# Kernel optimization log

Measured on AMD Instinct MI355X. Metric: run time of the kernel, lower is better.

## Reference

```python
import jax, jax.numpy as jnp
import numpy as np

N = 100000   # nodes
E = 1600000  # edges (avg degree 16)
IN = 64
HID = 16     # hardcoded in ChebNet.conv1
OUT = 40
K = 3


def setup_inputs() -> dict:
    key = jax.random.key(0)
    k0, k1, k2, k3 = jax.random.split(key, 4)
    x = jax.random.normal(k0, (N, IN), jnp.float32)
    edge_index = jax.random.randint(k1, (2, E), 0, N, jnp.int32)
    # Glorot-style init for the K per-order linear maps of each ChebConv
    s1 = float(np.sqrt(2.0 / (IN + HID)))
    W1 = jax.random.normal(k2, (K, IN, HID), jnp.float32) * s1
    b1 = jnp.zeros((HID,), jnp.float32)
    s2 = float(np.sqrt(2.0 / (HID + OUT)))
    W2 = jax.random.normal(k3, (K, HID, OUT), jnp.float32) * s2
    b2 = jnp.zeros((OUT,), jnp.float32)
    return {"x": x, "edge_index": edge_index, "W1": W1, "b1": b1, "W2": W2, "b2": b2}


def cheb_conv(x, edge_index, W, b):
    """PyG ChebConv with normalization='sym', lambda_max=2.
    Scaled Laplacian: L_hat = 2L/lambda_max - I = -D^{-1/2} A D^{-1/2} (diag 0).
    out = sum_k T_k(L_hat) x @ W[k] + b, T0=x, T1=L_hat x, Tk=2 L_hat T_{k-1}-T_{k-2}.
    """
    row, col = edge_index[0], edge_index[1]
    ones = jnp.ones((edge_index.shape[1],), x.dtype)
    deg = jax.ops.segment_sum(ones, row, num_segments=N)
    dis = jnp.where(deg > 0, jax.lax.rsqrt(jnp.maximum(deg, 1.0)), 0.0)
    norm = -(dis[row] * dis[col])  # [E]

    def Lhat(z):  # sparse scatter-gather: gather src rows, scale, scatter-add to dst
        return jax.ops.segment_sum(norm[:, None] * z[row], col, num_segments=N)

    Tx0 = x
    out = Tx0 @ W[0]
    Tx1 = Lhat(x)
    if W.shape[0] > 1:
        out = out + Tx1 @ W[1]
    for k in range(2, W.shape[0]):
        Tx2 = 2.0 * Lhat(Tx1) - Tx0
        out = out + Tx2 @ W[k]
        Tx0, Tx1 = Tx1, Tx2
    return out + b


def reference(x, edge_index, W1, b1, W2, b2):
    h = jax.nn.relu(cheb_conv(x, edge_index, W1, b1))
    h = cheb_conv(h, edge_index, W2, b2)
    return jax.nn.log_softmax(h, axis=1)
```

## Files before the change

### kernel.cpp

```cpp
#include <hip/hip_runtime.h>
#include <hip/hip_bf16.h>


typedef unsigned short u16;

constexpr int N_    = 100000;
constexpr int E_    = 1600000;
constexpr int IN_   = 64;
constexpr int HID_  = 16;
constexpr int OUT_  = 40;
constexpr int CAP_  = 48;
constexpr int S_    = 64;
constexpr int EPS_  = E_ / S_;
constexpr int P4_   = 4;
constexpr int NPP4_ = N_ / P4_;
constexpr int P8_   = 8;
constexpr int NPP8_ = N_ / P8_;
constexpr int NPAD_ = 100352;

__device__ __forceinline__ float bf2f(u16 u) {
    return __uint_as_float((unsigned)u << 16);
}
__device__ __forceinline__ u16 f2bf(float x) {
    unsigned u = __float_as_uint(x);
    return (u16)((u + 0x7FFFu + ((u >> 16) & 1u)) >> 16);
}

__global__ void __launch_bounds__(1024)
hist2(const int* __restrict__ row, const int* __restrict__ col,
      u16* __restrict__ prow, u16* __restrict__ pcol) {
    __shared__ int lds[NPP4_];
    if (blockIdx.x < P4_ * S_) {
        int p = blockIdx.x & 3, s = blockIdx.x >> 2;
        for (int i = threadIdx.x; i < NPP4_; i += 1024) lds[i] = 0;
        __syncthreads();
        int lo = p * NPP4_, e0 = s * EPS_;
        for (int i = threadIdx.x; i < EPS_; i += 1024) {
            int c = col[e0 + i];
            unsigned d = (unsigned)(c - lo);
            if (d < (unsigned)NPP4_) atomicAdd(&lds[d], 1);
        }
        __syncthreads();
        u16* dst = pcol + (size_t)(p * S_ + s) * NPP4_;
        for (int i = threadIdx.x; i < NPP4_; i += 1024) dst[i] = (u16)lds[i];
    } else {
        int b = blockIdx.x - P4_ * S_;
        int p = b & 7, s = b >> 3;
        for (int i = threadIdx.x; i < NPP8_; i += 1024) lds[i] = 0;
        __syncthreads();
        int lo = p * NPP8_, e0 = s * EPS_;
        for (int i = threadIdx.x; i < EPS_; i += 1024) {
            int r = row[e0 + i];
            unsigned d = (unsigned)(r - lo);
            if (d < (unsigned)NPP8_) atomicAdd(&lds[d], 1);
        }
        __syncthreads();
        u16* dst = prow + (size_t)(p * S_ + s) * NPP8_;
        for (int i = threadIdx.x; i < NPP8_; i += 1024) dst[i] = (u16)lds[i];
    }
}

__global__ void __launch_bounds__(1024)
reduce_all(const u16* __restrict__ prow, const u16* __restrict__ pcol,
           float* __restrict__ dis, u16* __restrict__ pre, int* __restrict__ indeg) {
    int n = blockIdx.x * 1024 + threadIdx.x;
    if (n >= N_) return;
    {
        int p = n / NPP8_, i = n - p * NPP8_;
        const u16* base = prow + (size_t)(p * S_) * NPP8_ + i;
        int d = 0;
#pragma unroll 8
        for (int s = 0; s < S_; ++s) d += base[(size_t)s * NPP8_];
        dis[n] = (d > 0) ? rsqrtf((float)d) : 0.0f;
    }
    {
        int p = n / NPP4_, i = n - p * NPP4_;
        const u16* base = pcol + (size_t)(p * S_) * NPP4_ + i;
        int run = 0;
#pragma unroll 8
        for (int s = 0; s < S_; ++s) {
            pre[(size_t)s * NPAD_ + n] = (u16)run;
            run += base[(size_t)s * NPP4_];
        }
        indeg[n] = run;
    }
}

__global__ void __launch_bounds__(1024)
place_proj(const int* __restrict__ row, const int* __restrict__ col,
           const float* __restrict__ x, const float* __restrict__ W,
           const float* __restrict__ dis, const u16* __restrict__ pre,
           int* __restrict__ bucket,
           float* __restrict__ P0f, float* __restrict__ P2f,
           u16* __restrict__ A1, u16* __restrict__ A2) {
    __shared__ int pos[NPP4_];
    __shared__ float w[3 * IN_ * HID_];
    if (blockIdx.x < P4_ * S_) {
        int p = blockIdx.x & 3, s = blockIdx.x >> 2;
        int lo = p * NPP4_, e0 = s * EPS_;
        const u16* psrc = pre + (size_t)s * NPAD_ + lo;
        for (int i = threadIdx.x; i < NPP4_; i += 1024) pos[i] = psrc[i];
        __syncthreads();
        for (int i = threadIdx.x; i < EPS_; i += 1024) {
            int c = col[e0 + i];
            unsigned d = (unsigned)(c - lo);
            if (d < (unsigned)NPP4_) {
                int r = row[e0 + i];
                int q = atomicAdd(&pos[d], 1);
                if (q < CAP_) bucket[(size_t)c * CAP_ + q] = r;
            }
        }
    } else {
        for (int i = threadIdx.x; i < 3 * IN_ * HID_; i += 1024) w[i] = W[i];
        __syncthreads();
        int t = (blockIdx.x - P4_ * S_) * 1024 + threadIdx.x;
        if (t >= N_ * HID_) return;
        int n = t >> 4, j = t & 15;
        const float* xr = x + (size_t)n * IN_;
        float a0 = 0.f, a1 = 0.f, a2 = 0.f;
#pragma unroll
        for (int i = 0; i < IN_; ++i) {
            float xv = xr[i];
            a0 += xv * w[i * 16 + j];
            a1 += xv * w[1024 + i * 16 + j];
            a2 += xv * w[2048 + i * 16 + j];
        }
        float dn = dis[n];
        P0f[t] = a0;
        P2f[t] = a2;
        A1[t] = f2bf(dn * a1);
        A2[t] = f2bf(dn * a2);
    }
}

__global__ void g32b(const u16* __restrict__ A1, const u16* __restrict__ A2,
                     const int* __restrict__ indeg, const int* __restrict__ bucket,
                     const float* __restrict__ dis,
                     float* __restrict__ LP1f, u16* __restrict__ B2) {
    int wib = threadIdx.x >> 6, lane = threadIdx.x & 63;
    int n0 = (blockIdx.x * 4 + wib) * 4;
    int eg = lane >> 3, sub = lane & 7;
    const u16* Z = (sub < 4) ? A1 : A2;
    int fq = sub & 3;
    int4 mi = *(const int4*)&indeg[n0];
    int m[4] = {min(mi.x, CAP_), min(mi.y, CAP_), min(mi.z, CAP_), min(mi.w, CAP_)};
    int mmax = max(max(m[0], m[1]), max(m[2], m[3]));
    float ax[4] = {0,0,0,0}, ay[4] = {0,0,0,0}, az[4] = {0,0,0,0}, aw[4] = {0,0,0,0};
    for (int base = 0; base < mmax; base += 8) {
        int e = base + eg;
        int rr[4]; float vm[4];
#pragma unroll
        for (int k = 0; k < 4; ++k) {
            bool v = e < m[k];
            rr[k] = bucket[(size_t)(n0 + k) * CAP_ + (v ? e : 0)];
            vm[k] = v ? 1.0f : 0.0f;
        }
#pragma unroll
        for (int k = 0; k < 4; ++k) {
            int r = (vm[k] != 0.0f) ? rr[k] : 0;
            ushort4 zv = *(const ushort4*)&Z[(size_t)r * 16 + fq * 4];
            ax[k] += vm[k] * bf2f(zv.x); ay[k] += vm[k] * bf2f(zv.y);
            az[k] += vm[k] * bf2f(zv.z); aw[k] += vm[k] * bf2f(zv.w);
        }
    }
#pragma unroll
    for (int off = 8; off < 64; off <<= 1) {
#pragma unroll
        for (int k = 0; k < 4; ++k) {
            ax[k] += __shfl_xor(ax[k], off, 64); ay[k] += __shfl_xor(ay[k], off, 64);
            az[k] += __shfl_xor(az[k], off, 64); aw[k] += __shfl_xor(aw[k], off, 64);
        }
    }
    if (lane < 8) {
#pragma unroll
        for (int k = 0; k < 4; ++k) {
            int n = n0 + k;
            float dn = dis[n];
            if (lane < 4) {
                float4 v = {-dn * ax[k], -dn * ay[k], -dn * az[k], -dn * aw[k]};
                *(float4*)&LP1f[(size_t)n * 16 + fq * 4] = v;
            } else {
                float s = -(dn * dn);
                ushort4 v = {f2bf(s * ax[k]), f2bf(s * ay[k]),
                             f2bf(s * az[k]), f2bf(s * aw[k])};
                *(ushort4*)&B2[(size_t)n * 16 + fq * 4] = v;
            }
        }
    }
}

__device__ __forceinline__ void g16core4(const u16* __restrict__ Z,
                                         const int* __restrict__ indeg,
                                         const int* __restrict__ bucket,
                                         int n0, int lane, float4 acc[4]) {
    int eg = lane >> 2, fq = lane & 3;
    int4 mi = *(const int4*)&indeg[n0];
    int m[4] = {min(mi.x, CAP_), min(mi.y, CAP_), min(mi.z, CAP_), min(mi.w, CAP_)};
    int mmax = max(max(m[0], m[1]), max(m[2], m[3]));
    float ax[4] = {0,0,0,0}, ay[4] = {0,0,0,0}, az[4] = {0,0,0,0}, aw[4] = {0,0,0,0};
    for (int base = 0; base < mmax; base += 16) {
        int e = base + eg;
        int rr[4]; float vm[4];
#pragma unroll
        for (int k = 0; k < 4; ++k) {
            bool v = e < m[k];
            rr[k] = bucket[(size_t)(n0 + k) * CAP_ + (v ? e : 0)];
            vm[k] = v ? 1.0f : 0.0f;
        }
#pragma unroll
        for (int k = 0; k < 4; ++k) {
            int r = (vm[k] != 0.0f) ? rr[k] : 0;
            ushort4 zv = *(const ushort4*)&Z[(size_t)r * 16 + fq * 4];
            ax[k] += vm[k] * bf2f(zv.x); ay[k] += vm[k] * bf2f(zv.y);
            az[k] += vm[k] * bf2f(zv.z); aw[k] += vm[k] * bf2f(zv.w);
        }
    }
#pragma unroll
    for (int off = 4; off < 64; off <<= 1) {
#pragma unroll
        for (int k = 0; k < 4; ++k) {
            ax[k] += __shfl_xor(ax[k], off, 64); ay[k] += __shfl_xor(ay[k], off, 64);
            az[k] += __shfl_xor(az[k], off, 64); aw[k] += __shfl_xor(aw[k], off, 64);
        }
    }
#pragma unroll
    for (int k = 0; k < 4; ++k) {
        float4 r4 = {ax[k], ay[k], az[k], aw[k]};
        acc[k] = r4;
    }
}

__global__ void g16_combine(const u16* __restrict__ B2, const int* __restrict__ indeg,
                            const int* __restrict__ bucket, const float* __restrict__ dis,
                            const float* __restrict__ LP1f, const float* __restrict__ P2f,
                            const float* __restrict__ b1,
                            float* p0h , u16* __restrict__ Hs) {
    int wib = threadIdx.x >> 6, lane = threadIdx.x & 63;
    int n0 = (blockIdx.x * 4 + wib) * 4;
    float4 acc[4];
    g16core4(B2, indeg, bucket, n0, lane, acc);
    if (lane < 4) {
#pragma unroll
        for (int k = 0; k < 4; ++k) {
            int n = n0 + k;
            float dn = dis[n];
            float4 p0 = *(const float4*)&p0h[(size_t)n * 16 + lane * 4];
            float4 lp = *(const float4*)&LP1f[(size_t)n * 16 + lane * 4];
            float4 p2 = *(const float4*)&P2f[(size_t)n * 16 + lane * 4];
            float4 bb = *(const float4*)&b1[lane * 4];
            float4 hv;
            hv.x = fmaxf(p0.x + lp.x - 2.f * dn * acc[k].x - p2.x + bb.x, 0.f);
            hv.y = fmaxf(p0.y + lp.y - 2.f * dn * acc[k].y - p2.y + bb.y, 0.f);
            hv.z = fmaxf(p0.z + lp.z - 2.f * dn * acc[k].z - p2.z + bb.z, 0.f);
            hv.w = fmaxf(p0.w + lp.w - 2.f * dn * acc[k].w - p2.w + bb.w, 0.f);
            *(float4*)&p0h[(size_t)n * 16 + lane * 4] = hv;
            ushort4 hs = {f2bf(dn * hv.x), f2bf(dn * hv.y),
                          f2bf(dn * hv.z), f2bf(dn * hv.w)};
            *(ushort4*)&Hs[(size_t)n * 16 + lane * 4] = hs;
        }
    }
}

__global__ void g16_t1(const u16* __restrict__ Hs, const int* __restrict__ indeg,
                       const int* __restrict__ bucket, const float* __restrict__ dis,
                       float* __restrict__ T1f, u16* __restrict__ Ts) {
    int wib = threadIdx.x >> 6, lane = threadIdx.x & 63;
    int n0 = (blockIdx.x * 4 + wib) * 4;
    float4 acc[4];
    g16core4(Hs, indeg, bucket, n0, lane, acc);
    if (lane < 4) {
#pragma unroll
        for (int k = 0; k < 4; ++k) {
            int n = n0 + k;
            float dn = dis[n];
            float4 t1 = {-dn * acc[k].x, -dn * acc[k].y, -dn * acc[k].z, -dn * acc[k].w};
            *(float4*)&T1f[(size_t)n * 16 + lane * 4] = t1;
            ushort4 ts = {f2bf(dn * t1.x), f2bf(dn * t1.y),
                          f2bf(dn * t1.z), f2bf(dn * t1.w)};
            *(ushort4*)&Ts[(size_t)n * 16 + lane * 4] = ts;
        }
    }
}

__global__ void g16_t2(const u16* __restrict__ Ts, const int* __restrict__ indeg,
                       const int* __restrict__ bucket, const float* __restrict__ dis,
                       const float* __restrict__ Hf, float* __restrict__ T2f) {
    int wib = threadIdx.x >> 6, lane = threadIdx.x & 63;
    int n0 = (blockIdx.x * 4 + wib) * 4;
    float4 acc[4];
    g16core4(Ts, indeg, bucket, n0, lane, acc);
    if (lane < 4) {
#pragma unroll
        for (int k = 0; k < 4; ++k) {
            int n = n0 + k;
            float dn = dis[n];
            float4 h4 = *(const float4*)&Hf[(size_t)n * 16 + lane * 4];
            float4 t2;
            t2.x = -2.f * dn * acc[k].x - h4.x;
            t2.y = -2.f * dn * acc[k].y - h4.y;
            t2.z = -2.f * dn * acc[k].z - h4.z;
            t2.w = -2.f * dn * acc[k].w - h4.w;
            *(float4*)&T2f[(size_t)n * 16 + lane * 4] = t2;
        }
    }
}

__global__ void __launch_bounds__(256)
mm2_lsm(const float* __restrict__ Hf, const float* __restrict__ T1f,
        const float* __restrict__ T2f, const float* __restrict__ W2,
        const float* __restrict__ b2, float* __restrict__ out) {
    int n = blockIdx.x * 256 + threadIdx.x;
    if (n >= N_) return;
    float act[48];
#pragma unroll
    for (int q = 0; q < 4; ++q)
        *(float4*)&act[q * 4] = *(const float4*)&Hf[(size_t)n * 16 + q * 4];
#pragma unroll
    for (int q = 0; q < 4; ++q)
        *(float4*)&act[16 + q * 4] = *(const float4*)&T1f[(size_t)n * 16 + q * 4];
#pragma unroll
    for (int q = 0; q < 4; ++q)
        *(float4*)&act[32 + q * 4] = *(const float4*)&T2f[(size_t)n * 16 + q * 4];
    float acc[OUT_];
#pragma unroll
    for (int o = 0; o < OUT_; ++o) acc[o] = b2[o];
#pragma unroll
    for (int j = 0; j < HID_; ++j) {
        float a0 = act[j], a1 = act[16 + j], a2 = act[32 + j];
#pragma unroll
        for (int o = 0; o < OUT_; ++o) {
            acc[o] += a0 * W2[j * OUT_ + o]
                    + a1 * W2[640 + j * OUT_ + o]
                    + a2 * W2[1280 + j * OUT_ + o];
        }
    }
    float mx = acc[0];
#pragma unroll
    for (int o = 1; o < OUT_; ++o) mx = fmaxf(mx, acc[o]);
    float s = 0.f;
#pragma unroll
    for (int o = 0; o < OUT_; ++o) s += __expf(acc[o] - mx);
    float ls = mx + logf(s);
#pragma unroll
    for (int q = 0; q < 10; ++q) {
        float4 v = {acc[q * 4] - ls, acc[q * 4 + 1] - ls,
                    acc[q * 4 + 2] - ls, acc[q * 4 + 3] - ls};
        *(float4*)&out[(size_t)n * OUT_ + q * 4] = v;
    }
}


extern "C" void kernel_launch(void* const* d_in, const int* in_sizes, int n_in,
                              void* d_out, int out_size, void* d_ws, size_t ws_size,
                              hipStream_t stream) {
    const float* x  = (const float*)d_in[0];
    const int*   ei = (const int*)d_in[1];
    const float* W1 = (const float*)d_in[2];
    const float* b1 = (const float*)d_in[3];
    const float* W2 = (const float*)d_in[4];
    const float* b2 = (const float*)d_in[5];
    float* out = (float*)d_out;

    const int* row = ei;
    const int* col = ei + E_;

    char* wp = (char*)d_ws;
    float* dis    = (float*)wp;  wp += 401408;
    int*   indeg  = (int*)wp;    wp += 401408;
    int*   bucket = (int*)wp;    wp += (size_t)N_ * CAP_ * 4;
    u16*   pre    = (u16*)wp;    wp += (size_t)S_ * NPAD_ * 2;
    char*  region = wp;
    u16* pcol = (u16*)region;
    u16* prow = (u16*)(region + 12800000);
    wp = region;
    u16*   A1   = (u16*)wp;   wp += 3211264;
    u16*   A2   = (u16*)wp;   wp += 3211264;
    u16*   B2   = (u16*)wp;   wp += 3211264;
    float* P0f  = (float*)wp; wp += 6422528;
    float* P2f  = (float*)wp; wp += 6422528;
    float* LP1f = (float*)wp; wp += 6422528;

    float* Hf  = P0f;
    u16*   Hs  = A1;
    float* T1f = LP1f;
    u16*   Ts  = A2;
    float* T2f = P2f;

    hist2<<<P4_ * S_ + P8_ * S_, 1024, 0, stream>>>(row, col, prow, pcol);
    reduce_all<<<NPAD_ / 1024, 1024, 0, stream>>>(prow, pcol, dis, pre, indeg);
    place_proj<<<P4_ * S_ + 1563, 1024, 0, stream>>>(row, col, x, W1, dis, pre,
                                                     bucket, P0f, P2f, A1, A2);

    g32b<<<N_ / 16, 256, 0, stream>>>(A1, A2, indeg, bucket, dis, LP1f, B2);
    g16_combine<<<N_ / 16, 256, 0, stream>>>(B2, indeg, bucket, dis, LP1f, P2f, b1,
                                             P0f , Hs);
    g16_t1<<<N_ / 16, 256, 0, stream>>>(Hs, indeg, bucket, dis, T1f, Ts);
    g16_t2<<<N_ / 16, 256, 0, stream>>>(Ts, indeg, bucket, dis, Hf, T2f);
    mm2_lsm<<<(N_ + 255) / 256, 256, 0, stream>>>(Hf, T1f, T2f, W2, b2, out);
}
```

Before: 313.7 us.

## Unify row/col histogram partitioning and interleave bucket placement with projection blocks

The row-degree histogram now uses the same 4-way node partition as the column histogram, so hist2 has a single code path and launches 512 blocks instead of 768. In place_proj, bucket-placement blocks and projection blocks are interleaved by block index (bit 2 of blockIdx selects the role), so the slow atomic scatter blocks are spread across the grid instead of all sitting at the front. The weight buffer reuses the pos LDS array rather than declaring a separate shared array. The aim is better load balance and occupancy. The cost is 3128 launched blocks with some exiting early, plus fewer, larger per-block histograms for the row pass.

New measurement: 317.3 us. About the same (+1.2%).

```diff
diff --git a/kernel.cpp b/kernel.cpp
--- a/kernel.cpp
+++ b/kernel.cpp
@@ -14,9 +14,8 @@
 constexpr int EPS_  = E_ / S_;
 constexpr int P4_   = 4;
 constexpr int NPP4_ = N_ / P4_;
-constexpr int P8_   = 8;
-constexpr int NPP8_ = N_ / P8_;
 constexpr int NPAD_ = 100352;
+constexpr int PROJB_ = 1563;
 
 __device__ __forceinline__ float bf2f(u16 u) {
     return __uint_as_float((unsigned)u << 16);
@@ -30,34 +29,22 @@
 hist2(const int* __restrict__ row, const int* __restrict__ col,
       u16* __restrict__ prow, u16* __restrict__ pcol) {
     __shared__ int lds[NPP4_];
-    if (blockIdx.x < P4_ * S_) {
-        int p = blockIdx.x & 3, s = blockIdx.x >> 2;
-        for (int i = threadIdx.x; i < NPP4_; i += 1024) lds[i] = 0;
-        __syncthreads();
-        int lo = p * NPP4_, e0 = s * EPS_;
-        for (int i = threadIdx.x; i < EPS_; i += 1024) {
-            int c = col[e0 + i];
-            unsigned d = (unsigned)(c - lo);
-            if (d < (unsigned)NPP4_) atomicAdd(&lds[d], 1);
-        }
-        __syncthreads();
-        u16* dst = pcol + (size_t)(p * S_ + s) * NPP4_;
-        for (int i = threadIdx.x; i < NPP4_; i += 1024) dst[i] = (u16)lds[i];
-    } else {
-        int b = blockIdx.x - P4_ * S_;
-        int p = b & 7, s = b >> 3;
-        for (int i = threadIdx.x; i < NPP8_; i += 1024) lds[i] = 0;
-        __syncthreads();
-        int lo = p * NPP8_, e0 = s * EPS_;
-        for (int i = threadIdx.x; i < EPS_; i += 1024) {
-            int r = row[e0 + i];
-            unsigned d = (unsigned)(r - lo);
-            if (d < (unsigned)NPP8_) atomicAdd(&lds[d], 1);
-        }
-        __syncthreads();
-        u16* dst = prow + (size_t)(p * S_ + s) * NPP8_;
-        for (int i = threadIdx.x; i < NPP8_; i += 1024) dst[i] = (u16)lds[i];
-    }
+    bool isCol = blockIdx.x < P4_ * S_;
+    int b = isCol ? blockIdx.x : (blockIdx.x - P4_ * S_);
+    const int* arr = isCol ? col : row;
+    u16* dstbase = isCol ? pcol : prow;
+    int p = b & 3, s = b >> 2;
+    for (int i = threadIdx.x; i < NPP4_; i += 1024) lds[i] = 0;
+    __syncthreads();
+    int lo = p * NPP4_, e0 = s * EPS_;
+    for (int i = threadIdx.x; i < EPS_; i += 1024) {
+        int v = arr[e0 + i];
+        unsigned d = (unsigned)(v - lo);
+        if (d < (unsigned)NPP4_) atomicAdd(&lds[d], 1);
+    }
+    __syncthreads();
+    u16* dst = dstbase + (size_t)(p * S_ + s) * NPP4_;
+    for (int i = threadIdx.x; i < NPP4_; i += 1024) dst[i] = (u16)lds[i];
 }
 
 __global__ void __launch_bounds__(1024)
@@ -65,16 +52,15 @@
            float* __restrict__ dis, u16* __restrict__ pre, int* __restrict__ indeg) {
     int n = blockIdx.x * 1024 + threadIdx.x;
     if (n >= N_) return;
+    int p = n / NPP4_, i = n - p * NPP4_;
     {
-        int p = n / NPP8_, i = n - p * NPP8_;
-        const u16* base = prow + (size_t)(p * S_) * NPP8_ + i;
+        const u16* base = prow + (size_t)(p * S_) * NPP4_ + i;
         int d = 0;
 #pragma unroll 8
-        for (int s = 0; s < S_; ++s) d += base[(size_t)s * NPP8_];
+        for (int s = 0; s < S_; ++s) d += base[(size_t)s * NPP4_];
         dis[n] = (d > 0) ? rsqrtf((float)d) : 0.0f;
     }
     {
-        int p = n / NPP4_, i = n - p * NPP4_;
         const u16* base = pcol + (size_t)(p * S_) * NPP4_ + i;
         int run = 0;
 #pragma unroll 8
@@ -94,9 +80,11 @@
            float* __restrict__ P0f, float* __restrict__ P2f,
            u16* __restrict__ A1, u16* __restrict__ A2) {
     __shared__ int pos[NPP4_];
-    __shared__ float w[3 * IN_ * HID_];
-    if (blockIdx.x < P4_ * S_) {
-        int p = blockIdx.x & 3, s = blockIdx.x >> 2;
+    float* w = (float*)pos;
+    if ((blockIdx.x & 4) == 0) {
+        int s = (int)(blockIdx.x >> 3);
+        if (s >= S_) return;
+        int p = blockIdx.x & 3;
         int lo = p * NPP4_, e0 = s * EPS_;
         const u16* psrc = pre + (size_t)s * NPAD_ + lo;
         for (int i = threadIdx.x; i < NPP4_; i += 1024) pos[i] = psrc[i];
@@ -111,19 +99,21 @@
             }
         }
     } else {
+        int j = (int)(blockIdx.x >> 3) * 4 + (int)(blockIdx.x & 3);
+        if (j >= PROJB_) return;
         for (int i = threadIdx.x; i < 3 * IN_ * HID_; i += 1024) w[i] = W[i];
         __syncthreads();
-        int t = (blockIdx.x - P4_ * S_) * 1024 + threadIdx.x;
+        int t = j * 1024 + threadIdx.x;
         if (t >= N_ * HID_) return;
-        int n = t >> 4, j = t & 15;
+        int n = t >> 4, jj = t & 15;
         const float* xr = x + (size_t)n * IN_;
         float a0 = 0.f, a1 = 0.f, a2 = 0.f;
 #pragma unroll
         for (int i = 0; i < IN_; ++i) {
             float xv = xr[i];
-            a0 += xv * w[i * 16 + j];
-            a1 += xv * w[1024 + i * 16 + j];
-            a2 += xv * w[2048 + i * 16 + j];
+            a0 += xv * w[i * 16 + jj];
+            a1 += xv * w[1024 + i * 16 + jj];
+            a2 += xv * w[2048 + i * 16 + jj];
         }
         float dn = dis[n];
         P0f[t] = a0;
@@ -386,10 +376,10 @@
     u16*   Ts  = A2;
     float* T2f = P2f;
 
-    hist2<<<P4_ * S_ + P8_ * S_, 1024, 0, stream>>>(row, col, prow, pcol);
+    hist2<<<2 * P4_ * S_, 1024, 0, stream>>>(row, col, prow, pcol);
     reduce_all<<<NPAD_ / 1024, 1024, 0, stream>>>(prow, pcol, dis, pre, indeg);
-    place_proj<<<P4_ * S_ + 1563, 1024, 0, stream>>>(row, col, x, W1, dis, pre,
-                                                     bucket, P0f, P2f, A1, A2);
+    place_proj<<<3128, 1024, 0, stream>>>(row, col, x, W1, dis, pre,
+                                          bucket, P0f, P2f, A1, A2);
 
     g32b<<<N_ / 16, 256, 0, stream>>>(A1, A2, indeg, bucket, dis, LP1f, B2);
     g16_combine<<<N_ / 16, 256, 0, stream>>>(B2, indeg, bucket, dis, LP1f, P2f, b1,
```
